# Performance work log

Measured on AMD Instinct MI355X. Metric: run time of the kernel, lower is better.

Reference implementation:

```python
import jax, jax.numpy as jnp
import numpy as np

NUM_HEADS = 16
EPS = 1e-6
CHUNK = 128  # chunk length for exact chunked-recurrent causal linear attention


def setup_inputs() -> dict:
    key = jax.random.key(0)
    ks = jax.random.split(key, 6)
    B, T, E = 4, 2048, 1024
    s = 0.02
    x = jax.random.normal(ks[0], (B, T, E), jnp.float32)
    Wq = jax.random.normal(ks[1], (E, E), jnp.float32) * s
    Wk = jax.random.normal(ks[2], (E, E), jnp.float32) * s
    Wv = jax.random.normal(ks[3], (E, E), jnp.float32) * s
    Wp = jax.random.normal(ks[4], (E, E), jnp.float32) * s
    bp = jnp.zeros((E,), jnp.float32)
    return {"x": x, "Wq": Wq, "Wk": Wk, "Wv": Wv, "Wp": Wp, "bp": bp}


def reference(x, Wq, Wk, Wv, Wp, bp):
    B, T, E = x.shape
    H = NUM_HEADS
    D = E // H
    N = T // CHUNK

    q = x @ Wq.T
    k = x @ Wk.T
    v = x @ Wv.T

    def split_heads(t):  # [B,T,E] -> [B,H,N,C,D]
        return t.reshape(B, T, H, D).transpose(0, 2, 1, 3).reshape(B, H, N, CHUNK, D)

    phi_q = jax.nn.elu(split_heads(q)) + 1.0
    phi_k = jax.nn.elu(split_heads(k)) + 1.0
    vh = split_heads(v)

    # per-chunk KV state and key-sum, then exclusive prefix over chunks
    kv = jnp.einsum('bhncd,bhnce->bhnde', phi_k, vh)        # [B,H,N,D,D]
    zk = phi_k.sum(axis=3)                                   # [B,H,N,D]
    S_prev = jnp.concatenate(
        [jnp.zeros_like(kv[:, :, :1]), jnp.cumsum(kv, axis=2)[:, :, :-1]], axis=2)
    Z_prev = jnp.concatenate(
        [jnp.zeros_like(zk[:, :, :1]), jnp.cumsum(zk, axis=2)[:, :, :-1]], axis=2)

    # intra-chunk causal part
    A = jnp.einsum('bhncd,bhnsd->bhncs', phi_q, phi_k)       # [B,H,N,C,C]
    mask = jnp.tril(jnp.ones((CHUNK, CHUNK), bool))
    A = jnp.where(mask, A, 0.0)

    num = (jnp.einsum('bhncs,bhnse->bhnce', A, vh)
           + jnp.einsum('bhncd,bhnde->bhnce', phi_q, S_prev))
    den = A.sum(-1) + jnp.einsum('bhncd,bhnd->bhnc', phi_q, Z_prev) + EPS
    y = num / den[..., None]                                  # [B,H,N,C,D]

    y = y.reshape(B, H, T, D).transpose(0, 2, 1, 3).reshape(B, T, E)
    return y @ Wp.T + bp
```

## Files before the change

### kernel.cpp

```cpp
#include <hip/hip_runtime.h>
#include <hip/hip_bf16.h>
#include <stdint.h>

#define T_LEN  2048
#define E_DIM  1024
#define BATCH  4
#define HEADS  16
#define HDIM   64
#define CHUNK_ 128
#define NCHUNK 16
#define EPS_   1e-6f

typedef __attribute__((ext_vector_type(8))) short bf16x8;
typedef __attribute__((ext_vector_type(4))) float f32x4;

__device__ __forceinline__ float b2f(__hip_bfloat16 h) { return __bfloat162float(h); }
__device__ __forceinline__ float bu2f(unsigned short u) {
  return __uint_as_float((unsigned)u << 16);
}
__device__ __forceinline__ unsigned short f2bu(float f) {
  __hip_bfloat16 h = __float2bfloat16(f);
  return *(unsigned short*)&h;
}
__device__ __forceinline__ void gld_lds16(const void* g, void* l) {
  __builtin_amdgcn_global_load_lds((const __attribute__((address_space(1))) void*)g,
                                   (__attribute__((address_space(3))) void*)l,
                                   16, 0, 0);
}

#define MFMA16(a, b, c) __builtin_amdgcn_mfma_f32_16x16x32_bf16((a), (b), (c), 0, 0, 0)

__global__ __launch_bounds__(256)
void cast5(const float* __restrict__ x,  const float* __restrict__ w0,
           const float* __restrict__ w1, const float* __restrict__ w2,
           const float* __restrict__ w3,
           __hip_bfloat16* __restrict__ xb,  __hip_bfloat16* __restrict__ w0b,
           __hip_bfloat16* __restrict__ w1b, __hip_bfloat16* __restrict__ w2b,
           __hip_bfloat16* __restrict__ w3b)
{
  const int b = blockIdx.x;
  const float* s;
  __hip_bfloat16* d;
  size_t off;
  if (b < 8192) { s = x; d = xb; off = (size_t)b * 1024; }
  else {
    const int i = (b - 8192) >> 10;
    const int r = (b - 8192) & 1023;
    s = (i == 0) ? w0 : (i == 1) ? w1 : (i == 2) ? w2 : w3;
    d = (i == 0) ? w0b : (i == 1) ? w1b : (i == 2) ? w2b : w3b;
    off = (size_t)r * 1024;
  }
  const int t = threadIdx.x;
  float4 v = *(const float4*)(s + off + (size_t)t * 4);
  ushort4 o;
  o.x = f2bu(v.x); o.y = f2bu(v.y); o.z = f2bu(v.z); o.w = f2bu(v.w);
  *(ushort4*)((unsigned short*)d + off + (size_t)t * 4) = o;
}

__device__ __forceinline__ void gemm128_core(
    const __hip_bfloat16* __restrict__ X,
    const __hip_bfloat16* __restrict__ W,
    int bm, int bn, f32x4 acc[4][4],
    __hip_bfloat16* Xs, __hip_bfloat16* Ws)
{
  const int t = threadIdx.x, lane = t & 63, wave = t >> 6;
  const int wm = (wave >> 1) * 64, wn = (wave & 1) * 64;
  for (int k0 = 0; k0 < 1024; k0 += 32) {
    if (k0) __syncthreads();
#pragma unroll
    for (int i = 0; i < 2; ++i) {
      const int j = wave * 2 + i;
      const int m = j * 16 + (lane >> 2);
      const int kg = lane & 3;
      gld_lds16(X + (size_t)(bm * 128 + m) * 1024 + k0 + kg * 8, (char*)Xs + j * 1024);
      gld_lds16(W + (size_t)(bn * 128 + m) * 1024 + k0 + kg * 8, (char*)Ws + j * 1024);
    }
    __syncthreads();
    bf16x8 a[4], b[4];
#pragma unroll
    for (int i = 0; i < 4; ++i) {
      a[i] = *(const bf16x8*)&Xs[((wm + i * 16 + (lane & 15)) * 4 + (lane >> 4)) * 8];
      b[i] = *(const bf16x8*)&Ws[((wn + i * 16 + (lane & 15)) * 4 + (lane >> 4)) * 8];
    }
#pragma unroll
    for (int i = 0; i < 4; ++i)
#pragma unroll
      for (int jn = 0; jn < 4; ++jn)
        acc[i][jn] = MFMA16(a[i], b[jn], acc[i][jn]);
  }
}

__global__ __launch_bounds__(512, 1)
void gemm_qkv_v2(const __hip_bfloat16* __restrict__ X,
                 const __hip_bfloat16* __restrict__ Wq,
                 const __hip_bfloat16* __restrict__ Wk,
                 const __hip_bfloat16* __restrict__ Wv,
                 __hip_bfloat16* __restrict__ qo,
                 __hip_bfloat16* __restrict__ ko,
                 __hip_bfloat16* __restrict__ vo)
{
  __shared__ __align__(16) unsigned short As[3][8192];
  __shared__ __align__(16) unsigned short Bs[3][16384];

  const int bm = blockIdx.x;
  const int byy = blockIdx.y;
  const int which = byy >> 2, bn = byy & 3;
  const __hip_bfloat16* Wsel = (which == 0) ? Wq : (which == 1) ? Wk : Wv;
  __hip_bfloat16* Cc = (which == 0) ? qo : (which == 1) ? ko : vo;
  const bool elu = (which < 2);

  const int t = threadIdx.x, lane = t & 63, wv = t >> 6;
  const int wm = (wv >> 2) * 64;
  const int wn = (wv & 3) * 64;

  const __hip_bfloat16* Xp = X + (size_t)(bm * 128) * 1024;
  const __hip_bfloat16* Wp = Wsel + (size_t)(bn * 256) * 1024;

  const int lo    = (lane & 15) * 128;
  const int lohi0 = lo + (((lane >> 4)    ) ^ (lane & 7)) * 16;
  const int lohi1 = lo + (((lane >> 4) | 4) ^ (lane & 7)) * 16;
  const int srow = lane >> 3;
  const int scg  = (lane & 7) ^ (lane >> 3);

  auto stA = [&](int buf, int k0) {
#pragma unroll
    for (int ci = 0; ci < 2; ++ci) {
      const int row0 = (wv * 2 + ci) * 8;
      gld_lds16(Xp + (size_t)(row0 + srow) * 1024 + k0 + scg * 8,
                (char*)&As[buf][0] + row0 * 128);
    }
  };
  auto stB0 = [&](int buf, int k0) {
#pragma unroll
    for (int ci = 0; ci < 2; ++ci) {
      const int row0 = (wv * 2 + ci) * 8;
      gld_lds16(Wp + (size_t)(row0 + srow) * 1024 + k0 + scg * 8,
                (char*)&Bs[buf][0] + row0 * 128);
    }
  };
  auto stB1 = [&](int buf, int k0) {
#pragma unroll
    for (int ci = 0; ci < 2; ++ci) {
      const int row0 = 128 + (wv * 2 + ci) * 8;
      gld_lds16(Wp + (size_t)(row0 + srow) * 1024 + k0 + scg * 8,
                (char*)&Bs[buf][0] + row0 * 128);
    }
  };
  auto rdA = [&](int buf, int half, bf16x8 (&d)[2][2]) {
#pragma unroll
    for (int m = 0; m < 2; ++m) {
      const int rb = wm + half * 32 + m * 16;
      d[m][0] = *(const bf16x8*)((const char*)&As[buf][0] + rb * 128 + lohi0);
      d[m][1] = *(const bf16x8*)((const char*)&As[buf][0] + rb * 128 + lohi1);
    }
  };
  auto rdB = [&](int buf, int half, bf16x8 (&d)[2][2]) {
#pragma unroll
    for (int n = 0; n < 2; ++n) {
      const int rb = wn + half * 32 + n * 16;
      d[n][0] = *(const bf16x8*)((const char*)&Bs[buf][0] + rb * 128 + lohi0);
      d[n][1] = *(const bf16x8*)((const char*)&Bs[buf][0] + rb * 128 + lohi1);
    }
  };

  f32x4 acc[4][4];
#pragma unroll
  for (int m = 0; m < 4; ++m)
#pragma unroll
    for (int n = 0; n < 4; ++n) acc[m][n] = (f32x4){0.f, 0.f, 0.f, 0.f};

  bf16x8 Aa01[2][2], Ab01[2][2], Aa23[2][2], Ab23[2][2];
  bf16x8 Ba01[2][2], Bb01[2][2], Ba23[2][2], Bb23[2][2];

  stA(0, 0);  stB0(0, 0);  stB1(0, 0);
  stA(1, 64); stB0(1, 64); stB1(1, 64);
  asm volatile("s_waitcnt vmcnt(6)" ::: "memory");
  __builtin_amdgcn_s_barrier();
  __builtin_amdgcn_sched_barrier(0);
  rdA(0, 0, Aa01); rdB(0, 0, Ab01); rdA(0, 1, Aa23); rdB(0, 1, Ab23);

  auto qstep = [&](int j, int c,
                   bf16x8 (&ca01)[2][2], bf16x8 (&cb01)[2][2],
                   bf16x8 (&ca23)[2][2], bf16x8 (&cb23)[2][2],
                   bf16x8 (&na01)[2][2], bf16x8 (&nb01)[2][2],
                   bf16x8 (&na23)[2][2], bf16x8 (&nb23)[2][2]) {
    const int stg  = (c + 2 >= 3) ? c - 1 : c + 2;
    const int nbuf = (c + 1 >= 3) ? 0 : c + 1;
    const int k0n  = (j + 2) * 64;
    const bool dost = (j < 14);

    __builtin_amdgcn_s_setprio(1);
#pragma unroll
    for (int m = 0; m < 2; ++m)
#pragma unroll
      for (int n = 0; n < 2; ++n) {
        acc[m][n] = MFMA16(ca01[m][0], cb01[n][0], acc[m][n]);
        acc[m][n] = MFMA16(ca01[m][1], cb01[n][1], acc[m][n]);
      }
    __builtin_amdgcn_s_setprio(0);
    if (dost) stA(stg, k0n);

    __builtin_amdgcn_s_setprio(1);
#pragma unroll
    for (int m = 0; m < 2; ++m)
#pragma unroll
      for (int n = 0; n < 2; ++n) {
        acc[m][2 + n] = MFMA16(ca01[m][0], cb23[n][0], acc[m][2 + n]);
        acc[m][2 + n] = MFMA16(ca01[m][1], cb23[n][1], acc[m][2 + n]);
      }
    __builtin_amdgcn_s_setprio(0);
    if (dost) stB0(stg, k0n);

    __builtin_amdgcn_s_setprio(1);
#pragma unroll
    for (int m = 0; m < 2; ++m)
#pragma unroll
      for (int n = 0; n < 2; ++n) {
        acc[2 + m][n] = MFMA16(ca23[m][0], cb01[n][0], acc[2 + m][n]);
        acc[2 + m][n] = MFMA16(ca23[m][1], cb01[n][1], acc[2 + m][n]);
      }
    __builtin_amdgcn_s_setprio(0);
    if (dost) stB1(stg, k0n);

    if (j == 14) asm volatile("s_waitcnt vmcnt(0)" ::: "memory");
    else         asm volatile("s_waitcnt vmcnt(6)" ::: "memory");
    __builtin_amdgcn_s_barrier();
    __builtin_amdgcn_sched_barrier(0);

    rdA(nbuf, 0, na01); rdB(nbuf, 0, nb01);

    __builtin_amdgcn_s_setprio(1);
#pragma unroll
    for (int m = 0; m < 2; ++m)
#pragma unroll
      for (int n = 0; n < 2; ++n) {
        acc[2 + m][2 + n] = MFMA16(ca23[m][0], cb23[n][0], acc[2 + m][2 + n]);
        acc[2 + m][2 + n] = MFMA16(ca23[m][1], cb23[n][1], acc[2 + m][2 + n]);
      }
    __builtin_amdgcn_s_setprio(0);

    rdA(nbuf, 1, na23); rdB(nbuf, 1, nb23);
  };

  int c = 0;
#pragma unroll 1
  for (int jj = 0; jj < 8; ++jj) {
    qstep(2 * jj, c, Aa01, Ab01, Aa23, Ab23, Ba01, Bb01, Ba23, Bb23);
    c = (c == 2) ? 0 : c + 1;
    qstep(2 * jj + 1, c, Ba01, Bb01, Ba23, Bb23, Aa01, Ab01, Aa23, Ab23);
    c = (c == 2) ? 0 : c + 1;
  }

  const int lm = lane & 15;
  const int r0 = (lane >> 4) * 4;
#pragma unroll
  for (int m = 0; m < 4; ++m) {
    const int row = bm * 128 + wm + m * 16 + r0;
#pragma unroll
    for (int n = 0; n < 4; ++n) {
      const int col = bn * 256 + wn + n * 16 + lm;
#pragma unroll
      for (int r = 0; r < 4; ++r) {
        float vv = acc[m][n][r];
        if (elu) vv = (vv > 0.f) ? (vv + 1.f) : __expf(vv);
        Cc[(size_t)(row + r) * 1024 + col] = __float2bfloat16(vv);
      }
    }
  }
}

__global__ __launch_bounds__(256, 2)
void gemm_out(const __hip_bfloat16* __restrict__ X,
              const __hip_bfloat16* __restrict__ W,
              const float* __restrict__ bias,
              float* __restrict__ C)
{
  __shared__ __align__(16) __hip_bfloat16 Xs[128 * 32];
  __shared__ __align__(16) __hip_bfloat16 Ws[128 * 32];
  const int bm = blockIdx.x, bn = blockIdx.y;
  f32x4 acc[4][4];
#pragma unroll
  for (int i = 0; i < 4; ++i)
#pragma unroll
    for (int j = 0; j < 4; ++j) acc[i][j] = (f32x4){0.f, 0.f, 0.f, 0.f};
  gemm128_core(X, W, bm, bn, acc, Xs, Ws);
  const int lane = threadIdx.x & 63, wave = threadIdx.x >> 6;
  const int wm = (wave >> 1) * 64, wn = (wave & 1) * 64;
  const int r0 = (lane >> 4) * 4;
#pragma unroll
  for (int mi = 0; mi < 4; ++mi)
#pragma unroll
    for (int ni = 0; ni < 4; ++ni) {
      const int row = bm * 128 + wm + mi * 16 + r0;
      const int col = bn * 128 + wn + ni * 16 + (lane & 15);
      const float bv = bias[col];
#pragma unroll
      for (int r = 0; r < 4; ++r)
        C[(size_t)(row + r) * 1024 + col] = acc[mi][ni][r] + bv;
    }
}

__global__ __launch_bounds__(256)
void chunk_kv(const __hip_bfloat16* __restrict__ Kp,
              const __hip_bfloat16* __restrict__ Vp,
              float* __restrict__ kvout, float* __restrict__ zkout,
              unsigned short* __restrict__ vimg)
{
  const int bid = blockIdx.x;
  const int n = bid & 15, h = (bid >> 4) & 15, b = bid >> 8;
  __shared__ __align__(16) __hip_bfloat16 ks[CHUNK_ * HDIM];
  __shared__ __align__(16) __hip_bfloat16 vs[CHUNK_ * HDIM];
  const size_t base = ((size_t)(b * T_LEN + n * CHUNK_)) * E_DIM + h * HDIM;
  const int t = threadIdx.x;
  for (int i = t; i < CHUNK_ * 8; i += 256) {
    int r = i >> 3, c = (i & 7) << 3;
    *(uint4*)&ks[r * HDIM + c] = *(const uint4*)(Kp + base + (size_t)r * E_DIM + c);
    *(uint4*)&vs[r * HDIM + c] = *(const uint4*)(Vp + base + (size_t)r * E_DIM + c);
  }
  __syncthreads();
  const int d0 = (t >> 4) << 2, e0 = (t & 15) << 2;
  const unsigned short* ksu = (const unsigned short*)ks;
  const unsigned short* vsu0 = (const unsigned short*)vs;
  float acc[4][4] = {{0.f}};
  float z[4] = {0.f, 0.f, 0.f, 0.f};
  for (int c = 0; c < CHUNK_; ++c) {
    ushort4 kq = *(const ushort4*)(ksu + c * HDIM + d0);
    ushort4 vq = *(const ushort4*)(vsu0 + c * HDIM + e0);
    float kv4[4], vv4[4];
    kv4[0] = bu2f(kq.x); kv4[1] = bu2f(kq.y); kv4[2] = bu2f(kq.z); kv4[3] = bu2f(kq.w);
    vv4[0] = bu2f(vq.x); vv4[1] = bu2f(vq.y); vv4[2] = bu2f(vq.z); vv4[3] = bu2f(vq.w);
#pragma unroll
    for (int i = 0; i < 4; ++i) {
      z[i] += kv4[i];
#pragma unroll
      for (int j = 0; j < 4; ++j) acc[i][j] += kv4[i] * vv4[j];
    }
  }
  float* o = kvout + (size_t)bid * (HDIM * HDIM);
  const int dg = d0 >> 3, doff = d0 & 7;
#pragma unroll
  for (int i = 0; i < 4; ++i)
#pragma unroll
    for (int j = 0; j < 4; ++j)
      o[dg * 512 + (e0 + j) * 8 + doff + i] = acc[i][j];
  if (e0 == 0) {
#pragma unroll
    for (int i = 0; i < 4; ++i) zkout[(size_t)bid * HDIM + d0 + i] = z[i];
  }
  const unsigned short* vsu = (const unsigned short*)vs;
  unsigned short* vo = vimg + (size_t)bid * 8192;
  for (int slot = t; slot < 1024; slot += 256) {
    const int sg = slot >> 6, e = slot & 63;
    ushort4 lo, hi;
    lo.x = vsu[(sg * 8 + 0) * 64 + e]; lo.y = vsu[(sg * 8 + 1) * 64 + e];
    lo.z = vsu[(sg * 8 + 2) * 64 + e]; lo.w = vsu[(sg * 8 + 3) * 64 + e];
    hi.x = vsu[(sg * 8 + 4) * 64 + e]; hi.y = vsu[(sg * 8 + 5) * 64 + e];
    hi.z = vsu[(sg * 8 + 6) * 64 + e]; hi.w = vsu[(sg * 8 + 7) * 64 + e];
    *(ushort4*)&vo[slot * 8] = lo;
    *(ushort4*)&vo[slot * 8 + 4] = hi;
  }
}

__global__ __launch_bounds__(256)
void prefix_chunks(float* __restrict__ S, float* __restrict__ Z)
{
  const int bh = blockIdx.x >> 2, seg = blockIdx.x & 3;
  const int t = threadIdx.x;
  float* base = S + (size_t)bh * NCHUNK * (HDIM * HDIM) + seg * 1024 + t * 4;
  float4 v[NCHUNK];
#pragma unroll
  for (int n = 0; n < NCHUNK; ++n)
    v[n] = *(const float4*)(base + (size_t)n * (HDIM * HDIM));
  float4 run = {0.f, 0.f, 0.f, 0.f};
#pragma unroll
  for (int n = 0; n < NCHUNK; ++n) {
    *(float4*)(base + (size_t)n * (HDIM * HDIM)) = run;
    run.x += v[n].x; run.y += v[n].y; run.z += v[n].z; run.w += v[n].w;
  }
  if (seg == 0 && t < 16) {
    float* zb = Z + (size_t)bh * NCHUNK * HDIM + t * 4;
    float4 zv[NCHUNK];
#pragma unroll
    for (int n = 0; n < NCHUNK; ++n) zv[n] = *(const float4*)(zb + n * HDIM);
    float4 zr = {0.f, 0.f, 0.f, 0.f};
#pragma unroll
    for (int n = 0; n < NCHUNK; ++n) {
      *(float4*)(zb + n * HDIM) = zr;
      zr.x += zv[n].x; zr.y += zv[n].y; zr.z += zv[n].z; zr.w += zv[n].w;
    }
  }
}

#define PW_STRIDE 136

__global__ __launch_bounds__(256, 3)
void chunk_attn(const __hip_bfloat16* __restrict__ Qp,
                const __hip_bfloat16* __restrict__ Kp,
                const unsigned short* __restrict__ vimg,
                const float* __restrict__ Simg,
                const float* __restrict__ Zp,
                __hip_bfloat16* __restrict__ Yp)
{
  __shared__ __align__(16) unsigned short VL[8192];
  __shared__ __align__(16) unsigned short SL[4096];
  __shared__ __align__(16) unsigned short PL[4 * 16 * PW_STRIDE];

  const int bid = blockIdx.x;
  const int n = bid & 15, h = (bid >> 4) & 15, b = bid >> 8;
  const int tokbase = b * T_LEN + n * CHUNK_;
  const size_t gbase = (size_t)tokbase * E_DIM + h * HDIM;
  const int t = threadIdx.x, lane = t & 63, wv = t >> 6;
  const int lm = lane & 15, kg = lane >> 4;

#pragma unroll
  for (int i = 0; i < 4; ++i) {
    const int j = wv * 4 + i;
    gld_lds16(vimg + (size_t)bid * 8192 + (size_t)(j * 64 + lane) * 8,
              (char*)VL + j * 1024);
  }
#pragma unroll
  for (int i = 0; i < 4; ++i) {
    const int idx = i * 1024 + t * 4;
    float4 s4 = *(const float4*)(Simg + (size_t)bid * 4096 + idx);
    ushort4 o;
    o.x = f2bu(s4.x); o.y = f2bu(s4.y); o.z = f2bu(s4.z); o.w = f2bu(s4.w);
    *(ushort4*)&SL[idx] = o;
  }

  const int mts[2] = { wv, 7 - wv };
  bf16x8 aq[2][2];
#pragma unroll
  for (int mi = 0; mi < 2; ++mi)
#pragma unroll
    for (int kh = 0; kh < 2; ++kh)
      aq[mi][kh] = *(const bf16x8*)(Qp + gbase +
                    (size_t)(mts[mi] * 16 + lm) * E_DIM + kh * 32 + kg * 8);
  bf16x8 zb[2];
#pragma unroll
  for (int kh = 0; kh < 2; ++kh) {
    float4 z0 = *(const float4*)(Zp + (size_t)bid * 64 + kh * 32 + kg * 8);
    float4 z1 = *(const float4*)(Zp + (size_t)bid * 64 + kh * 32 + kg * 8 + 4);
    zb[kh][0] = (short)f2bu(z0.x); zb[kh][1] = (short)f2bu(z0.y);
    zb[kh][2] = (short)f2bu(z0.z); zb[kh][3] = (short)f2bu(z0.w);
    zb[kh][4] = (short)f2bu(z1.x); zb[kh][5] = (short)f2bu(z1.y);
    zb[kh][6] = (short)f2bu(z1.z); zb[kh][7] = (short)f2bu(z1.w);
  }

  __syncthreads();

  f32x4 accn[2][4];
  f32x4 accden[2];
#pragma unroll
  for (int mi = 0; mi < 2; ++mi) {
    accden[mi] = (f32x4){EPS_, EPS_, EPS_, EPS_};
#pragma unroll
    for (int ne = 0; ne < 4; ++ne) accn[mi][ne] = (f32x4){0.f, 0.f, 0.f, 0.f};
  }

#pragma unroll
  for (int mi = 0; mi < 2; ++mi)
#pragma unroll
    for (int kh = 0; kh < 2; ++kh) {
      const bf16x8 a = aq[mi][kh];
      accden[mi] = MFMA16(a, zb[kh], accden[mi]);
#pragma unroll
      for (int ne = 0; ne < 4; ++ne) {
        bf16x8 bs = *(const bf16x8*)&SL[((kh * 4 + kg) * 64 + ne * 16 + lm) * 8];
        accn[mi][ne] = MFMA16(a, bs, accn[mi][ne]);
      }
    }

  unsigned short* Pw = PL + wv * 16 * PW_STRIDE;
  bf16x8 ones;
#pragma unroll
  for (int j = 0; j < 8; ++j) ones[j] = (short)0x3F80;

#pragma unroll
  for (int mi = 0; mi < 2; ++mi) {
    const int mt = mts[mi], m0 = mt * 16;
    for (int nt = 0; nt <= mt; ++nt) {
      f32x4 pt = (f32x4){0.f, 0.f, 0.f, 0.f};
#pragma unroll
      for (int kh = 0; kh < 2; ++kh) {
        bf16x8 ak = *(const bf16x8*)(Kp + gbase +
                     (size_t)(nt * 16 + lm) * E_DIM + kh * 32 + kg * 8);
        pt = MFMA16(ak, aq[mi][kh], pt);
      }
      unsigned short u[4];
#pragma unroll
      for (int r = 0; r < 4; ++r) {
        float v = pt[r];
        if (nt == mt) {
          v = ((kg * 4 + r) <= lm) ? v : 0.f;
        }
        u[r] = f2bu(v);
      }
      const int sidx = lm * PW_STRIDE + nt * 16 + kg * 4;
      *(unsigned*)&Pw[sidx]     = (unsigned)u[0] | ((unsigned)u[1] << 16);
      *(unsigned*)&Pw[sidx + 2] = (unsigned)u[2] | ((unsigned)u[3] << 16);
    }
    if ((mt & 1) == 0 && lane < 32) {
      const int m = lane >> 1, half = lane & 1;
      *(uint4*)&Pw[m * PW_STRIDE + (mt + 1) * 16 + half * 8] = (uint4){0u, 0u, 0u, 0u};
    }
    const int ktc = (mt + 2) >> 1;
    for (int kt = 0; kt < ktc; ++kt) {
      bf16x8 ap = *(const bf16x8*)&Pw[lm * PW_STRIDE + kt * 32 + kg * 8];
      accden[mi] = MFMA16(ap, ones, accden[mi]);
#pragma unroll
      for (int ne = 0; ne < 4; ++ne) {
        bf16x8 bv = *(const bf16x8*)&VL[((kt * 4 + kg) * 64 + ne * 16 + lm) * 8];
        accn[mi][ne] = MFMA16(ap, bv, accn[mi][ne]);
      }
    }
  }

#pragma unroll
  for (int mi = 0; mi < 2; ++mi) {
    const int m0 = mts[mi] * 16;
    float inv[4];
#pragma unroll
    for (int r = 0; r < 4; ++r) inv[r] = 1.f / accden[mi][r];
#pragma unroll
    for (int ne = 0; ne < 4; ++ne) {
      const int col = h * HDIM + ne * 16 + lm;
#pragma unroll
      for (int r = 0; r < 4; ++r) {
        const int row = tokbase + m0 + kg * 4 + r;
        Yp[(size_t)row * E_DIM + col] = __float2bfloat16(accn[mi][ne][r] * inv[r]);
      }
    }
  }
}

extern "C" void kernel_launch(void* const* d_in, const int* in_sizes, int n_in,
                              void* d_out, int out_size, void* d_ws, size_t ws_size,
                              hipStream_t stream)
{
  const float* x  = (const float*)d_in[0];
  const float* Wq = (const float*)d_in[1];
  const float* Wk = (const float*)d_in[2];
  const float* Wv = (const float*)d_in[3];
  const float* Wp = (const float*)d_in[4];
  const float* bp = (const float*)d_in[5];
  float* out = (float*)d_out;

  const size_t MT = (size_t)BATCH * T_LEN;
  char* w = (char*)d_ws;
  __hip_bfloat16* xb  = (__hip_bfloat16*)w; w += MT * E_DIM * sizeof(__hip_bfloat16);
  __hip_bfloat16* Wqb = (__hip_bfloat16*)w; w += (size_t)E_DIM * E_DIM * sizeof(__hip_bfloat16);
  __hip_bfloat16* Wkb = (__hip_bfloat16*)w; w += (size_t)E_DIM * E_DIM * sizeof(__hip_bfloat16);
  __hip_bfloat16* Wvb = (__hip_bfloat16*)w; w += (size_t)E_DIM * E_DIM * sizeof(__hip_bfloat16);
  __hip_bfloat16* Wpb = (__hip_bfloat16*)w; w += (size_t)E_DIM * E_DIM * sizeof(__hip_bfloat16);
  __hip_bfloat16* q = (__hip_bfloat16*)w; w += MT * E_DIM * sizeof(__hip_bfloat16);
  __hip_bfloat16* k = (__hip_bfloat16*)w; w += MT * E_DIM * sizeof(__hip_bfloat16);
  __hip_bfloat16* v = (__hip_bfloat16*)w; w += MT * E_DIM * sizeof(__hip_bfloat16);
  __hip_bfloat16* y = (__hip_bfloat16*)w; w += MT * E_DIM * sizeof(__hip_bfloat16);
  float* S = (float*)w; w += (size_t)BATCH * HEADS * NCHUNK * HDIM * HDIM * sizeof(float);
  float* Z = (float*)w; w += (size_t)BATCH * HEADS * NCHUNK * HDIM * sizeof(float);
  unsigned short* vimg = (unsigned short*)xb;

  cast5<<<8192 + 4096, 256, 0, stream>>>(x, Wq, Wk, Wv, Wp, xb, Wqb, Wkb, Wvb, Wpb);
  gemm_qkv_v2<<<dim3(64, 12), 512, 0, stream>>>(xb, Wqb, Wkb, Wvb, q, k, v);
  chunk_kv<<<BATCH * HEADS * NCHUNK, 256, 0, stream>>>(k, v, S, Z, vimg);
  prefix_chunks<<<BATCH * HEADS * 4, 256, 0, stream>>>(S, Z);
  chunk_attn<<<BATCH * HEADS * NCHUNK, 256, 0, stream>>>(q, k, vimg, S, Z, y);
  gemm_out<<<dim3(MT / 128, 8), 256, 0, stream>>>(y, Wpb, bp, out);
}
```

Measured before the change: 234.0 us.

## Shrink QKV GEMM K-tile for higher occupancy; reuse pipelined GEMM for output projection

The QKV projection kernel now uses a 32-wide K step with half-size LDS triple buffers and an adjusted XOR swizzle, and declares 4 blocks per CU in its launch bounds. This is meant to let more waves overlap memory and MFMA. The output projection drops the simple 128x128 single-buffer GEMM in favour of the triple-buffered, prio-scheduled 128x256 pipeline that the QKV kernel used before. Risks are register pressure at the higher occupancy target, and fewer blocks (256) in the output GEMM, which may underfill the GPU.

```diff
diff --git a/kernel.cpp b/kernel.cpp
--- a/kernel.cpp
+++ b/kernel.cpp
@@ -57,41 +57,8 @@
   *(ushort4*)((unsigned short*)d + off + (size_t)t * 4) = o;
 }
 
-__device__ __forceinline__ void gemm128_core(
-    const __hip_bfloat16* __restrict__ X,
-    const __hip_bfloat16* __restrict__ W,
-    int bm, int bn, f32x4 acc[4][4],
-    __hip_bfloat16* Xs, __hip_bfloat16* Ws)
-{
-  const int t = threadIdx.x, lane = t & 63, wave = t >> 6;
-  const int wm = (wave >> 1) * 64, wn = (wave & 1) * 64;
-  for (int k0 = 0; k0 < 1024; k0 += 32) {
-    if (k0) __syncthreads();
-#pragma unroll
-    for (int i = 0; i < 2; ++i) {
-      const int j = wave * 2 + i;
-      const int m = j * 16 + (lane >> 2);
-      const int kg = lane & 3;
-      gld_lds16(X + (size_t)(bm * 128 + m) * 1024 + k0 + kg * 8, (char*)Xs + j * 1024);
-      gld_lds16(W + (size_t)(bn * 128 + m) * 1024 + k0 + kg * 8, (char*)Ws + j * 1024);
-    }
-    __syncthreads();
-    bf16x8 a[4], b[4];
-#pragma unroll
-    for (int i = 0; i < 4; ++i) {
-      a[i] = *(const bf16x8*)&Xs[((wm + i * 16 + (lane & 15)) * 4 + (lane >> 4)) * 8];
-      b[i] = *(const bf16x8*)&Ws[((wn + i * 16 + (lane & 15)) * 4 + (lane >> 4)) * 8];
-    }
-#pragma unroll
-    for (int i = 0; i < 4; ++i)
-#pragma unroll
-      for (int jn = 0; jn < 4; ++jn)
-        acc[i][jn] = MFMA16(a[i], b[jn], acc[i][jn]);
-  }
-}
-
-__global__ __launch_bounds__(512, 1)
-void gemm_qkv_v2(const __hip_bfloat16* __restrict__ X,
+__global__ __launch_bounds__(512, 4)
+void gemm_qkv_v4(const __hip_bfloat16* __restrict__ X,
                  const __hip_bfloat16* __restrict__ Wq,
                  const __hip_bfloat16* __restrict__ Wk,
                  const __hip_bfloat16* __restrict__ Wv,
@@ -99,8 +66,8 @@
                  __hip_bfloat16* __restrict__ ko,
                  __hip_bfloat16* __restrict__ vo)
 {
-  __shared__ __align__(16) unsigned short As[3][8192];
-  __shared__ __align__(16) unsigned short Bs[3][16384];
+  __shared__ __align__(16) unsigned short As[3][4096];
+  __shared__ __align__(16) unsigned short Bs[3][8192];
 
   const int bm = blockIdx.x;
   const int byy = blockIdx.y;
@@ -115,6 +82,142 @@
 
   const __hip_bfloat16* Xp = X + (size_t)(bm * 128) * 1024;
   const __hip_bfloat16* Wp = Wsel + (size_t)(bn * 256) * 1024;
+
+  const int lohi = (lane & 15) * 64 + (((lane >> 4) ^ ((lane >> 1) & 3)) * 16);
+  const int srow = lane >> 2;
+  const int scg  = (lane & 3) ^ ((lane >> 3) & 3);
+
+  auto stA = [&](int buf, int k0) {
+    const int row0 = wv * 16;
+    gld_lds16(Xp + (size_t)(row0 + srow) * 1024 + k0 + scg * 8,
+              (char*)&As[buf][0] + row0 * 64);
+  };
+  auto stB = [&](int buf, int k0, int u) {
+    const int row0 = u * 128 + wv * 16;
+    gld_lds16(Wp + (size_t)(row0 + srow) * 1024 + k0 + scg * 8,
+              (char*)&Bs[buf][0] + row0 * 64);
+  };
+  auto rdA = [&](int buf, bf16x8 (&d)[4]) {
+#pragma unroll
+    for (int m = 0; m < 4; ++m)
+      d[m] = *(const bf16x8*)((const char*)&As[buf][0] + (wm + m * 16) * 64 + lohi);
+  };
+  auto rdB = [&](int buf, bf16x8 (&d)[4]) {
+#pragma unroll
+    for (int n = 0; n < 4; ++n)
+      d[n] = *(const bf16x8*)((const char*)&Bs[buf][0] + (wn + n * 16) * 64 + lohi);
+  };
+
+  f32x4 acc[4][4];
+#pragma unroll
+  for (int m = 0; m < 4; ++m)
+#pragma unroll
+    for (int n = 0; n < 4; ++n) acc[m][n] = (f32x4){0.f, 0.f, 0.f, 0.f};
+
+  bf16x8 Xa[4], Xb[4], Ya[4], Yb[4];
+
+  stA(0, 0);  stB(0, 0, 0);  stB(0, 0, 1);
+  stA(1, 32); stB(1, 32, 0); stB(1, 32, 1);
+  asm volatile("s_waitcnt vmcnt(3)" ::: "memory");
+  __builtin_amdgcn_s_barrier();
+  __builtin_amdgcn_sched_barrier(0);
+  rdA(0, Xa); rdB(0, Xb);
+
+  auto qstep = [&](int j, int c,
+                   bf16x8 (&ca)[4], bf16x8 (&cb)[4],
+                   bf16x8 (&na)[4], bf16x8 (&nb)[4]) {
+    const int stg  = (c + 2 >= 3) ? c - 1 : c + 2;
+    const int nbuf = (c + 1 >= 3) ? 0 : c + 1;
+    const int k0n  = (j + 2) * 32;
+    const bool dost = (j < 30);
+
+    __builtin_amdgcn_s_setprio(1);
+#pragma unroll
+    for (int m = 0; m < 2; ++m)
+#pragma unroll
+      for (int n = 0; n < 2; ++n) acc[m][n] = MFMA16(ca[m], cb[n], acc[m][n]);
+    __builtin_amdgcn_s_setprio(0);
+    if (dost) stA(stg, k0n);
+
+    __builtin_amdgcn_s_setprio(1);
+#pragma unroll
+    for (int m = 0; m < 2; ++m)
+#pragma unroll
+      for (int n = 0; n < 2; ++n) acc[m][2 + n] = MFMA16(ca[m], cb[2 + n], acc[m][2 + n]);
+    __builtin_amdgcn_s_setprio(0);
+    if (dost) stB(stg, k0n, 0);
+
+    __builtin_amdgcn_s_setprio(1);
+#pragma unroll
+    for (int m = 0; m < 2; ++m)
+#pragma unroll
+      for (int n = 0; n < 2; ++n) acc[2 + m][n] = MFMA16(ca[2 + m], cb[n], acc[2 + m][n]);
+    __builtin_amdgcn_s_setprio(0);
+    if (dost) stB(stg, k0n, 1);
+
+    if (j >= 30) asm volatile("s_waitcnt vmcnt(0)" ::: "memory");
+    else         asm volatile("s_waitcnt vmcnt(3)" ::: "memory");
+    __builtin_amdgcn_s_barrier();
+    __builtin_amdgcn_sched_barrier(0);
+
+    rdA(nbuf, na);
+
+    __builtin_amdgcn_s_setprio(1);
+#pragma unroll
+    for (int m = 0; m < 2; ++m)
+#pragma unroll
+      for (int n = 0; n < 2; ++n)
+        acc[2 + m][2 + n] = MFMA16(ca[2 + m], cb[2 + n], acc[2 + m][2 + n]);
+    __builtin_amdgcn_s_setprio(0);
+
+    rdB(nbuf, nb);
+  };
+
+  int c = 0;
+#pragma unroll 1
+  for (int jj = 0; jj < 16; ++jj) {
+    qstep(2 * jj, c, Xa, Xb, Ya, Yb);
+    c = (c == 2) ? 0 : c + 1;
+    qstep(2 * jj + 1, c, Ya, Yb, Xa, Xb);
+    c = (c == 2) ? 0 : c + 1;
+  }
+
+  const int lm = lane & 15;
+  const int r0 = (lane >> 4) * 4;
+#pragma unroll
+  for (int m = 0; m < 4; ++m) {
+    const int row = bm * 128 + wm + m * 16 + r0;
+#pragma unroll
+    for (int n = 0; n < 4; ++n) {
+      const int col = bn * 256 + wn + n * 16 + lm;
+#pragma unroll
+      for (int r = 0; r < 4; ++r) {
+        float vv = acc[m][n][r];
+        if (elu) vv = (vv > 0.f) ? (vv + 1.f) : __expf(vv);
+        Cc[(size_t)(row + r) * 1024 + col] = __float2bfloat16(vv);
+      }
+    }
+  }
+}
+
+__global__ __launch_bounds__(512, 1)
+void gemm_out_v2(const __hip_bfloat16* __restrict__ X,
+                 const __hip_bfloat16* __restrict__ W,
+                 const float* __restrict__ bias,
+                 float* __restrict__ C)
+{
+  __shared__ __align__(16) unsigned short As[3][8192];
+  __shared__ __align__(16) unsigned short Bs[3][16384];
+
+  const int bm = blockIdx.x;
+  const int bn = blockIdx.y;
+
+  const int t = threadIdx.x, lane = t & 63, wv = t >> 6;
+  const int wm = (wv >> 2) * 64;
+  const int wn = (wv & 3) * 64;
+
+  const __hip_bfloat16* Xp = X + (size_t)(bm * 128) * 1024;
+  const __hip_bfloat16* Wp = W + (size_t)(bn * 256) * 1024;
 
   const int lo    = (lane & 15) * 128;
   const int lohi0 = lo + (((lane >> 4)    ) ^ (lane & 7)) * 16;
@@ -259,45 +362,12 @@
 #pragma unroll
     for (int n = 0; n < 4; ++n) {
       const int col = bn * 256 + wn + n * 16 + lm;
-#pragma unroll
-      for (int r = 0; r < 4; ++r) {
-        float vv = acc[m][n][r];
-        if (elu) vv = (vv > 0.f) ? (vv + 1.f) : __expf(vv);
-        Cc[(size_t)(row + r) * 1024 + col] = __float2bfloat16(vv);
-      }
-    }
-  }
-}
-
-__global__ __launch_bounds__(256, 2)
-void gemm_out(const __hip_bfloat16* __restrict__ X,
-              const __hip_bfloat16* __restrict__ W,
-              const float* __restrict__ bias,
-              float* __restrict__ C)
-{
-  __shared__ __align__(16) __hip_bfloat16 Xs[128 * 32];
-  __shared__ __align__(16) __hip_bfloat16 Ws[128 * 32];
-  const int bm = blockIdx.x, bn = blockIdx.y;
-  f32x4 acc[4][4];
-#pragma unroll
-  for (int i = 0; i < 4; ++i)
-#pragma unroll
-    for (int j = 0; j < 4; ++j) acc[i][j] = (f32x4){0.f, 0.f, 0.f, 0.f};
-  gemm128_core(X, W, bm, bn, acc, Xs, Ws);
-  const int lane = threadIdx.x & 63, wave = threadIdx.x >> 6;
-  const int wm = (wave >> 1) * 64, wn = (wave & 1) * 64;
-  const int r0 = (lane >> 4) * 4;
-#pragma unroll
-  for (int mi = 0; mi < 4; ++mi)
-#pragma unroll
-    for (int ni = 0; ni < 4; ++ni) {
-      const int row = bm * 128 + wm + mi * 16 + r0;
-      const int col = bn * 128 + wn + ni * 16 + (lane & 15);
       const float bv = bias[col];
 #pragma unroll
       for (int r = 0; r < 4; ++r)
-        C[(size_t)(row + r) * 1024 + col] = acc[mi][ni][r] + bv;
-    }
+        C[(size_t)(row + r) * 1024 + col] = acc[m][n][r] + bv;
+    }
+  }
 }
 
 __global__ __launch_bounds__(256)
@@ -561,9 +631,9 @@
   unsigned short* vimg = (unsigned short*)xb;
 
   cast5<<<8192 + 4096, 256, 0, stream>>>(x, Wq, Wk, Wv, Wp, xb, Wqb, Wkb, Wvb, Wpb);
-  gemm_qkv_v2<<<dim3(64, 12), 512, 0, stream>>>(xb, Wqb, Wkb, Wvb, q, k, v);
+  gemm_qkv_v4<<<dim3(64, 12), 512, 0, stream>>>(xb, Wqb, Wkb, Wvb, q, k, v);
   chunk_kv<<<BATCH * HEADS * NCHUNK, 256, 0, stream>>>(k, v, S, Z, vimg);
   prefix_chunks<<<BATCH * HEADS * 4, 256, 0, stream>>>(S, Z);
   chunk_attn<<<BATCH * HEADS * NCHUNK, 256, 0, stream>>>(q, k, vimg, S, Z, y);
-  gemm_out<<<dim3(MT / 128, 8), 256, 0, stream>>>(y, Wpb, bp, out);
-}
+  gemm_out_v2<<<dim3(64, 4), 512, 0, stream>>>(y, Wpb, bp, out);
+}
```

Result: no change. 237.1 us (+1.3%).
